# Kernel optimization log

Measured on AMD Instinct MI355X. Metric: run time of the kernel, lower is better.

## Reference

```python
import jax, jax.numpy as jnp
import numpy as np

D_MODEL = 1024
NUM_HEADS = 16
HEAD_DIM = D_MODEL // NUM_HEADS
THETA = 10000.0
BATCH = 2
SEQ = 2048


def _apply_rope(x, positions):
    # x: (b, h, s, hd), positions: (b, s) int
    hd = x.shape[-1]
    inv_freq = 1.0 / (THETA ** (jnp.arange(0, hd, 2, dtype=jnp.float32) / hd))  # (hd/2,)
    ang = positions.astype(jnp.float32)[:, None, :, None] * inv_freq  # (b,1,s,hd/2)
    cos, sin = jnp.cos(ang), jnp.sin(ang)
    x1 = x[..., 0::2]
    x2 = x[..., 1::2]
    r1 = x1 * cos - x2 * sin
    r2 = x1 * sin + x2 * cos
    return jnp.stack([r1, r2], axis=-1).reshape(x.shape)


def setup_inputs() -> dict:
    key = jax.random.key(0)
    ks = jax.random.split(key, 5)
    scale = 1.0 / np.sqrt(D_MODEL)
    x = jax.random.normal(ks[0], (BATCH, SEQ, D_MODEL), dtype=jnp.float32)
    token_positions = jnp.broadcast_to(jnp.arange(SEQ, dtype=jnp.int32), (BATCH, SEQ))
    W_q = jax.random.normal(ks[1], (D_MODEL, D_MODEL), dtype=jnp.float32) * scale
    W_k = jax.random.normal(ks[2], (D_MODEL, D_MODEL), dtype=jnp.float32) * scale
    W_v = jax.random.normal(ks[3], (D_MODEL, D_MODEL), dtype=jnp.float32) * scale
    W_o = jax.random.normal(ks[4], (D_MODEL, D_MODEL), dtype=jnp.float32) * scale
    return {"x": x, "token_positions": token_positions, "W_q": W_q, "W_k": W_k, "W_v": W_v, "W_o": W_o}


def reference(x, token_positions, W_q, W_k, W_v, W_o):
    b, s, _ = x.shape
    h, hd = NUM_HEADS, HEAD_DIM
    # bias-free Linear: y = x @ W^T, W: (out, in)
    def proj(W):
        return jnp.einsum('bsd,ed->bse', x, W).reshape(b, s, h, hd).transpose(0, 2, 1, 3)
    Q = _apply_rope(proj(W_q), token_positions)
    K = _apply_rope(proj(W_k), token_positions)
    V = proj(W_v)
    scores = jnp.einsum('bhqd,bhkd->bhqk', Q, K) / jnp.sqrt(jnp.float32(hd))
    causal = jnp.triu(jnp.full((s, s), -jnp.inf, dtype=scores.dtype), k=1)
    attn = jax.nn.softmax(scores + causal, axis=-1)
    Z = jnp.einsum('bhqk,bhkd->bhqd', attn, V)
    Z = Z.transpose(0, 2, 1, 3).reshape(b, s, h * hd)
    return jnp.einsum('bse,de->bsd', Z, W_o)
```

## Files before the change

kernel.cpp:

```cpp
#include <hip/hip_runtime.h>
#include <hip/hip_bf16.h>


#define BATCH 2
#define SEQ   2048
#define NH    16
#define HD    64
#define DM    1024
#define MTOT  (BATCH*SEQ)

typedef __attribute__((ext_vector_type(8))) short bf16x8;
typedef __attribute__((ext_vector_type(4))) float f32x4;
typedef __attribute__((ext_vector_type(4))) unsigned int u32x4;
typedef unsigned short u16;
typedef unsigned int   u32;

__device__ __forceinline__ float b2f(u16 h){ return __uint_as_float(((u32)h) << 16); }
__device__ __forceinline__ u16 f2b(float f){
  u32 u = __float_as_uint(f);
  u32 r = (u + 0x7FFFu + ((u >> 16) & 1u)) >> 16;
  return (u16)r;
}
__device__ __forceinline__ u16 cvt1(float f){
  __hip_bfloat16 h = __float2bfloat16(f);
  return *reinterpret_cast<u16*>(&h);
}
__device__ __forceinline__ u32 pk2(float lo, float hi){
  return (u32)cvt1(lo) | ((u32)cvt1(hi) << 16);
}
__device__ __forceinline__ f32x4 mfma16(bf16x8 a, bf16x8 b, f32x4 c){
  return __builtin_amdgcn_mfma_f32_16x16x32_bf16(a, b, c, 0, 0, 0);
}
__device__ __forceinline__ void gload_lds16(const u16* g, u16* l){
  __builtin_amdgcn_global_load_lds((const __attribute__((address_space(1))) unsigned int*)g,
                                   (__attribute__((address_space(3))) unsigned int*)l, 16, 0, 0);
}

__global__ __launch_bounds__(256) void cvt_all(const float* __restrict__ x,
    const float* __restrict__ wq, const float* __restrict__ wk,
    const float* __restrict__ wv, const float* __restrict__ wo,
    u16* __restrict__ xb, u16* __restrict__ wb)
{
  const long NX = (long)MTOT * DM;
  const long NW = (long)DM * DM;
  const long tot4 = (NX + 4*NW) >> 2;
  for (long t = (long)blockIdx.x*blockDim.x + threadIdx.x; t < tot4;
       t += (long)gridDim.x*blockDim.x){
    long e = t << 2;
    const float* s; u16* d;
    if (e < NX){ s = x + e; d = xb + e; }
    else {
      long j = e - NX; int z = (int)(j >> 20);
      const float* ws = (z==0)?wq:(z==1)?wk:(z==2)?wv:wo;
      s = ws + (j & (NW-1)); d = wb + j;
    }
    float4 v = *(const float4*)s;
    u32 lo = (u32)f2b(v.x) | ((u32)f2b(v.y) << 16);
    u32 hi = (u32)f2b(v.z) | ((u32)f2b(v.w) << 16);
    uint2 o; o.x = lo; o.y = hi;
    *(uint2*)d = o;
  }
}

__global__ __launch_bounds__(256) void rope_table(float2* __restrict__ tab){
  int t = blockIdx.x*blockDim.x + threadIdx.x;
  if (t >= SEQ*32) return;
  int s = t >> 5, i = t & 31;
  float inv = 1.0f / powf(10000.0f, (float)i * (1.0f/32.0f));
  float a = (float)s * inv;
  tab[t] = make_float2(cosf(a), sinf(a));
}

__device__ __forceinline__ void gemm128_core(const u16* __restrict__ A, const u16* __restrict__ B,
    int mbase, int nbase, u16* Alds, u16* Blds, f32x4 acc[4][4])
{
  const int tid = threadIdx.x;
  const int w = tid >> 6, l = tid & 63, g = l >> 4, c = l & 15;
  const int wr = (w >> 1)*64, wc = (w & 1)*64;
  const int srow = l >> 3;
  const int scol = ((l & 7) ^ srow)*8;
  const u16* Ag = A + (long)(mbase + w*32 + srow)*DM + scol;
  const u16* Bg = B + (long)(nbase + w*32 + srow)*DM + scol;
  u16* Alb = Alds + w*2048;
  u16* Blb = Blds + w*2048;

  for (int k0 = 0; k0 < DM; k0 += 64){
    __syncthreads();
    #pragma unroll
    for (int i = 0; i < 4; i++){
      gload_lds16(Ag + k0 + (long)(8*i)*DM, Alb + i*512);
      gload_lds16(Bg + k0 + (long)(8*i)*DM, Blb + i*512);
    }
    __syncthreads();
    #pragma unroll
    for (int ks = 0; ks < 2; ks++){
      bf16x8 af[4], bfr[4];
      #pragma unroll
      for (int mi = 0; mi < 4; mi++){
        int row = wr + mi*16 + c;
        af[mi] = *(const bf16x8*)&Alds[row*64 + (((ks*4 + g) ^ (row & 7))*8)];
      }
      #pragma unroll
      for (int nj = 0; nj < 4; nj++){
        int row = wc + nj*16 + c;
        bfr[nj] = *(const bf16x8*)&Blds[row*64 + (((ks*4 + g) ^ (row & 7))*8)];
      }
      #pragma unroll
      for (int mi = 0; mi < 4; mi++)
        #pragma unroll
        for (int nj = 0; nj < 4; nj++)
          acc[mi][nj] = mfma16(af[mi], bfr[nj], acc[mi][nj]);
    }
  }
}

__global__ __launch_bounds__(256) void gemm_qkv(const u16* __restrict__ xb,
                                                const u16* __restrict__ wb,
                                                u16* __restrict__ qkvr)
{
  __shared__ u16 Alds[128*64];
  __shared__ u16 Blds[128*64];
  const int z = blockIdx.z;
  const u16* Bm = wb + (long)z * DM * DM;
  u16* C = qkvr + (long)z * MTOT * DM;
  const int nbase = blockIdx.x*128, mbase = blockIdx.y*128;
  const int w = threadIdx.x >> 6, l = threadIdx.x & 63, g = l >> 4, c = l & 15;
  const int wr = (w >> 1)*64, wc = (w & 1)*64;
  f32x4 acc[4][4] = {};
  gemm128_core(xb, Bm, mbase, nbase, Alds, Blds, acc);
  #pragma unroll
  for (int mi = 0; mi < 4; mi++)
    #pragma unroll
    for (int nj = 0; nj < 4; nj++)
      #pragma unroll
      for (int r = 0; r < 4; r++){
        int row = mbase + wr + mi*16 + 4*g + r;
        int col = nbase + wc + nj*16 + c;
        C[(long)row*DM + col] = f2b(acc[mi][nj][r]);
      }
}

__global__ __launch_bounds__(256) void gemm_out(const u16* __restrict__ Zb,
                                                const u16* __restrict__ wob,
                                                float* __restrict__ out)
{
  __shared__ u16 Alds[128*64];
  __shared__ u16 Blds[128*64];
  const int nbase = blockIdx.x*128, mbase = blockIdx.y*128;
  const int w = threadIdx.x >> 6, l = threadIdx.x & 63, g = l >> 4, c = l & 15;
  const int wr = (w >> 1)*64, wc = (w & 1)*64;
  f32x4 acc[4][4] = {};
  gemm128_core(Zb, wob, mbase, nbase, Alds, Blds, acc);
  #pragma unroll
  for (int mi = 0; mi < 4; mi++)
    #pragma unroll
    for (int nj = 0; nj < 4; nj++)
      #pragma unroll
      for (int r = 0; r < 4; r++){
        int row = mbase + wr + mi*16 + 4*g + r;
        int col = nbase + wc + nj*16 + c;
        out[(long)row*DM + col] = acc[mi][nj][r];
      }
}

__global__ __launch_bounds__(256) void rope_scatter(const u16* __restrict__ qkvr,
    u16* __restrict__ Qd, u16* __restrict__ Kd, u16* __restrict__ Vt,
    const float2* __restrict__ tab, const int* __restrict__ pos)
{
  int st = blockIdx.x, h = blockIdx.y, b = blockIdx.z;
  int s0 = st*64;
  const u16* Qraw = qkvr;
  const u16* Kraw = qkvr + (long)MTOT*DM;
  const u16* Vraw = qkvr + 2L*MTOT*DM;
  const float SC = 0.125f * 1.44269504089f;

  for (int t = threadIdx.x; t < 64*32; t += 256){
    int sl = t >> 5, i = t & 31;
    int s = s0 + sl;
    int p = pos[b*SEQ + s];
    if (p < 0) p = 0; if (p >= SEQ) p = SEQ - 1;
    float2 cs = tab[p*32 + i];
    long inoff  = (long)(b*SEQ + s)*DM + h*HD + 2*i;
    long outoff = ((long)(b*NH + h)*SEQ + s)*HD + 2*i;
    u32 qe = *(const u32*)(Qraw + inoff);
    float x1 = b2f((u16)(qe & 0xffff)), x2 = b2f((u16)(qe >> 16));
    float r1 = (x1*cs.x - x2*cs.y)*SC;
    float r2 = (x1*cs.y + x2*cs.x)*SC;
    *(u32*)(Qd + outoff) = (u32)f2b(r1) | ((u32)f2b(r2) << 16);
    u32 ke = *(const u32*)(Kraw + inoff);
    x1 = b2f((u16)(ke & 0xffff)); x2 = b2f((u16)(ke >> 16));
    r1 = x1*cs.x - x2*cs.y;
    r2 = x1*cs.y + x2*cs.x;
    *(u32*)(Kd + outoff) = (u32)f2b(r1) | ((u32)f2b(r2) << 16);
  }

  __shared__ u16 vt[64][65];
  for (int t = threadIdx.x; t < 64*8; t += 256){
    int sl = t >> 3, ch = (t & 7)*8;
    bf16x8 v = *(const bf16x8*)(Vraw + (long)(b*SEQ + s0 + sl)*DM + h*HD + ch);
    #pragma unroll
    for (int j = 0; j < 8; j++) vt[sl][ch + j] = (u16)v[j];
  }
  __syncthreads();
  for (int t = threadIdx.x; t < 64*8; t += 256){
    int d = t >> 3, ch = (t & 7)*8;
    bf16x8 v;
    #pragma unroll
    for (int j = 0; j < 8; j++) v[j] = (short)vt[ch + j][d];
    *(bf16x8*)(Vt + ((long)(b*NH + h)*HD + d)*SEQ + s0 + ch) = v;
  }
}

__device__ __forceinline__ int kperm(int a){
  return (a & 32) | ((a & 4) << 2) | ((a & 24) >> 1) | (a & 3);
}

__global__ __launch_bounds__(256) void attn(const u16* __restrict__ Q, const u16* __restrict__ K,
                                            const u16* __restrict__ Vt,
                                            u16* __restrict__ Opart, float* __restrict__ Lsum)
{
  const int pair = (int)blockIdx.x >> 1;
  const int half = blockIdx.x & 1;
  const int h = blockIdx.y, b = blockIdx.z;
  const int tid = threadIdx.x, w = tid >> 6, l = tid & 63, g = l >> 4, c = l & 15;
  const u16* Kp = K  + (long)(b*NH + h)*SEQ*HD;
  const u16* Vp = Vt + (long)(b*NH + h)*HD*SEQ;

  __shared__ u16 K_lds[2][64][64];
  __shared__ u16 V_lds[2][64][64];

  const int srow0 = tid >> 3, sch = tid & 7;
  const int kpr0 = kperm(srow0), kpr1 = kperm(srow0 + 32);
  const int cswz = c & 7;

  bf16x8 ones;
  #pragma unroll
  for (int j = 0; j < 8; j++) ones[j] = (short)0x3F80;

  int cur = 0;
  #pragma unroll 1
  for (int seg = 0; seg < 2; ++seg){
    const int qt = seg ? (31 - pair) : pair;
    const int qbase = qt*64;
    const int qrow = qbase + w*16;
    const u16* Qp = Q + ((long)(b*NH + h)*SEQ + qrow)*HD;
    bf16x8 qf0 = *(const bf16x8*)(Qp + c*HD + g*8);
    bf16x8 qf1 = *(const bf16x8*)(Qp + c*HD + 32 + g*8);

    const int ntH0  = (qt + 2) >> 1;
    const int tstart = half ? ntH0 : 0;
    const int tend   = half ? (qt + 1) : ntH0;

    f32x4 accz[4] = {};
    f32x4 lacc = {};

    if (tstart < tend){
      __syncthreads();
      bf16x8 kr[2], vr[2];
      #pragma unroll
      for (int i = 0; i < 2; i++){
        int row = srow0 + i*32;
        kr[i] = *(const bf16x8*)(Kp + (long)(tstart*64 + row)*HD + sch*8);
        vr[i] = *(const bf16x8*)(Vp + (long)row*SEQ + tstart*64 + sch*8);
      }
      *(bf16x8*)&K_lds[cur][kpr0][(sch ^ (kpr0 & 7))*8] = kr[0];
      *(bf16x8*)&K_lds[cur][kpr1][(sch ^ (kpr1 & 7))*8] = kr[1];
      *(bf16x8*)&V_lds[cur][srow0][(sch ^ (srow0 & 7))*8] = vr[0];
      *(bf16x8*)&V_lds[cur][srow0+32][(sch ^ ((srow0+32) & 7))*8] = vr[1];

      for (int t = tstart; t < tend; ++t){
        const int kbase = t*64;
        __syncthreads();

        if (t < tend-1){
          const int nb = kbase + 64;
          #pragma unroll
          for (int i = 0; i < 2; i++){
            int row = srow0 + i*32;
            kr[i] = *(const bf16x8*)(Kp + (long)(nb + row)*HD + sch*8);
            vr[i] = *(const bf16x8*)(Vp + (long)row*SEQ + nb + sch*8);
          }
        }

        f32x4 s[4];
        __builtin_amdgcn_s_setprio(1);
        #pragma unroll
        for (int sub = 0; sub < 4; sub++){
          int row = sub*16 + c;
          bf16x8 ka0 = *(const bf16x8*)&K_lds[cur][row][((0+g) ^ cswz)*8];
          bf16x8 ka1 = *(const bf16x8*)&K_lds[cur][row][((4+g) ^ cswz)*8];
          f32x4 z4 = {};
          z4 = mfma16(ka0, qf0, z4);
          z4 = mfma16(ka1, qf1, z4);
          s[sub] = z4;
        }
        __builtin_amdgcn_s_setprio(0);

        const bool edge = (kbase + 63 > qrow);
        const int q = qrow + c;
        if (edge){
          #pragma unroll
          for (int sub = 0; sub < 4; sub++)
            #pragma unroll
            for (int r = 0; r < 4; r++){
              int key = kbase + ((sub >> 1) << 5) + 8*g + ((sub & 1) << 2) + r;
              if (key > q) s[sub][r] = -1e30f;
            }
        }
        #pragma unroll
        for (int sub = 0; sub < 4; sub++)
          #pragma unroll
          for (int r = 0; r < 4; r++)
            s[sub][r] = exp2f(s[sub][r]);

        u32x4 p0, p1;
        p0[0] = pk2(s[0][0], s[0][1]); p0[1] = pk2(s[0][2], s[0][3]);
        p0[2] = pk2(s[1][0], s[1][1]); p0[3] = pk2(s[1][2], s[1][3]);
        p1[0] = pk2(s[2][0], s[2][1]); p1[1] = pk2(s[2][2], s[2][3]);
        p1[2] = pk2(s[3][0], s[3][1]); p1[3] = pk2(s[3][2], s[3][3]);
        bf16x8 pf0 = __builtin_bit_cast(bf16x8, p0);
        bf16x8 pf1 = __builtin_bit_cast(bf16x8, p1);

        __builtin_amdgcn_s_setprio(1);
        lacc = mfma16(pf0, ones, lacc);
        lacc = mfma16(pf1, ones, lacc);
        #pragma unroll
        for (int dt = 0; dt < 4; dt++){
          int vrow = dt*16 + c;
          bf16x8 vf0 = *(const bf16x8*)&V_lds[cur][vrow][((0+g) ^ cswz)*8];
          bf16x8 vf1 = *(const bf16x8*)&V_lds[cur][vrow][((4+g) ^ cswz)*8];
          accz[dt] = mfma16(pf0, vf0, accz[dt]);
          accz[dt] = mfma16(pf1, vf1, accz[dt]);
        }
        __builtin_amdgcn_s_setprio(0);

        if (t < tend-1){
          int nx = cur ^ 1;
          *(bf16x8*)&K_lds[nx][kpr0][(sch ^ (kpr0 & 7))*8] = kr[0];
          *(bf16x8*)&K_lds[nx][kpr1][(sch ^ (kpr1 & 7))*8] = kr[1];
          *(bf16x8*)&V_lds[nx][srow0][(sch ^ (srow0 & 7))*8] = vr[0];
          *(bf16x8*)&V_lds[nx][srow0+32][(sch ^ ((srow0+32) & 7))*8] = vr[1];
          cur = nx;
        }
      }
    }

    const int pbase = (((b*NH + h)*32 + qt)*2 + half);
    if (c == 0){
      #pragma unroll
      for (int r = 0; r < 4; r++)
        Lsum[pbase*64 + w*16 + 4*g + r] = lacc[r];
    }
    u16* Op = Opart + (long)pbase*(64*64);
    #pragma unroll
    for (int dt = 0; dt < 4; dt++)
      #pragma unroll
      for (int r = 0; r < 4; r++)
        Op[(w*16 + 4*g + r)*64 + dt*16 + c] = cvt1(accz[dt][r]);
  }
}

__global__ __launch_bounds__(256) void attn_combine(const u16* __restrict__ Opart,
                                                    const float* __restrict__ Lsum,
                                                    u16* __restrict__ Z)
{
  const int qt = blockIdx.x, h = blockIdx.y, b = blockIdx.z;
  const int p0 = ((b*NH + h)*32 + qt)*2, p1 = p0 + 1;
  const int row = threadIdx.x >> 2;
  const int d0  = (threadIdx.x & 3)*16;
  float inv = 1.f / (Lsum[p0*64 + row] + Lsum[p1*64 + row]);
  const u16* o0 = Opart + ((long)p0*64 + row)*64 + d0;
  const u16* o1 = Opart + ((long)p1*64 + row)*64 + d0;
  const int s = qt*64 + row;
  u16* zp = Z + (long)(b*SEQ + s)*DM + h*HD + d0;
  #pragma unroll
  for (int j = 0; j < 2; j++){
    bf16x8 va = *(const bf16x8*)(o0 + j*8);
    bf16x8 vb = *(const bf16x8*)(o1 + j*8);
    bf16x8 ov;
    #pragma unroll
    for (int e = 0; e < 8; e++){
      float z = (b2f((u16)va[e]) + b2f((u16)vb[e]))*inv;
      ov[e] = (short)cvt1(z);
    }
    *(bf16x8*)(zp + j*8) = ov;
  }
}

extern "C" void kernel_launch(void* const* d_in, const int* in_sizes, int n_in,
                              void* d_out, int out_size, void* d_ws, size_t ws_size,
                              hipStream_t stream)
{
  const float* x  = (const float*)d_in[0];
  const int*   pos= (const int*)d_in[1];
  const float* wq = (const float*)d_in[2];
  const float* wk = (const float*)d_in[3];
  const float* wv = (const float*)d_in[4];
  const float* wo = (const float*)d_in[5];
  float* out = (float*)d_out;

  const long NX = (long)MTOT*DM;
  const long NW = (long)DM*DM;
  char* p = (char*)d_ws;
  u16* xb   = (u16*)p;  p += NX*2;
  u16* wb   = (u16*)p;  p += 4*NW*2;
  u16* qkvr = (u16*)p;  p += 3*NX*2;
  u16* Qd   = (u16*)p;  p += NX*2;
  u16* Kd   = (u16*)p;  p += NX*2;
  u16* Vt   = (u16*)p;  p += NX*2;
  u16* Zb   = (u16*)p;  p += NX*2;
  float2* tab = (float2*)p; p += (long)SEQ*32*sizeof(float2);
  u16* Opart = (u16*)p;  p += 2L*NX*2;
  float* Lsum = (float*)p; p += 2048L*64*sizeof(float);
  (void)ws_size; (void)n_in; (void)in_sizes; (void)out_size;

  hipLaunchKernelGGL(cvt_all,     dim3(2048),      dim3(256), 0, stream, x, wq, wk, wv, wo, xb, wb);
  hipLaunchKernelGGL(rope_table,  dim3(256),       dim3(256), 0, stream, tab);
  hipLaunchKernelGGL(gemm_qkv,    dim3(8,32,3),    dim3(256), 0, stream, xb, wb, qkvr);
  hipLaunchKernelGGL(rope_scatter,dim3(32,16,2),   dim3(256), 0, stream, qkvr, Qd, Kd, Vt, tab, pos);
  hipLaunchKernelGGL(attn,        dim3(32,16,2),   dim3(256), 0, stream, Qd, Kd, Vt, Opart, Lsum);
  hipLaunchKernelGGL(attn_combine,dim3(32,16,2),   dim3(256), 0, stream, Opart, Lsum, Zb);
  hipLaunchKernelGGL(gemm_out,    dim3(8,32),      dim3(256), 0, stream, Zb, wb + 3*NW, out);
}
```

Baseline: 124.6 us.

## Use 128x64 tiles for output GEMM and flatten attention LDS addressing

The output projection GEMM moves from 128x128 tiles to 128x64 tiles with its own inline direct-to-LDS load loop, doubling the grid from 256 to 512 blocks so more CUs are occupied on the 4096x1024 output. Separately, the attention kernel merges its K/V shared buffers into one flat array and uses precomputed offsets and pointer increments in place of per-iteration index arithmetic. The smaller GEMM tile lowers data reuse per block and raises total global traffic.

```diff
diff --git a/kernel.cpp b/kernel.cpp
--- a/kernel.cpp
+++ b/kernel.cpp
@@ -145,16 +145,52 @@
                                                 float* __restrict__ out)
 {
   __shared__ u16 Alds[128*64];
-  __shared__ u16 Blds[128*64];
-  const int nbase = blockIdx.x*128, mbase = blockIdx.y*128;
-  const int w = threadIdx.x >> 6, l = threadIdx.x & 63, g = l >> 4, c = l & 15;
-  const int wr = (w >> 1)*64, wc = (w & 1)*64;
-  f32x4 acc[4][4] = {};
-  gemm128_core(Zb, wob, mbase, nbase, Alds, Blds, acc);
+  __shared__ u16 Blds[64*64];
+  const int nbase = blockIdx.x*64, mbase = blockIdx.y*128;
+  const int tid = threadIdx.x;
+  const int w = tid >> 6, l = tid & 63, g = l >> 4, c = l & 15;
+  const int wr = (w >> 1)*64, wc = (w & 1)*32;
+  const int srow = l >> 3;
+  const int scol = ((l & 7) ^ srow)*8;
+  const u16* Ag = Zb  + (long)(mbase + w*32 + srow)*DM + scol;
+  const u16* Bg = wob + (long)(nbase + w*16 + srow)*DM + scol;
+  u16* Alb = Alds + w*2048;
+  u16* Blb = Blds + w*1024;
+  f32x4 acc[4][2] = {};
+
+  for (int k0 = 0; k0 < DM; k0 += 64){
+    __syncthreads();
+    #pragma unroll
+    for (int i = 0; i < 4; i++)
+      gload_lds16(Ag + k0 + (long)(8*i)*DM, Alb + i*512);
+    #pragma unroll
+    for (int i = 0; i < 2; i++)
+      gload_lds16(Bg + k0 + (long)(8*i)*DM, Blb + i*512);
+    __syncthreads();
+    #pragma unroll
+    for (int ks = 0; ks < 2; ks++){
+      bf16x8 af[4], bfr[2];
+      #pragma unroll
+      for (int mi = 0; mi < 4; mi++){
+        int row = wr + mi*16 + c;
+        af[mi] = *(const bf16x8*)&Alds[row*64 + (((ks*4 + g) ^ (row & 7))*8)];
+      }
+      #pragma unroll
+      for (int nj = 0; nj < 2; nj++){
+        int row = wc + nj*16 + c;
+        bfr[nj] = *(const bf16x8*)&Blds[row*64 + (((ks*4 + g) ^ (row & 7))*8)];
+      }
+      #pragma unroll
+      for (int mi = 0; mi < 4; mi++)
+        #pragma unroll
+        for (int nj = 0; nj < 2; nj++)
+          acc[mi][nj] = mfma16(af[mi], bfr[nj], acc[mi][nj]);
+    }
+  }
   #pragma unroll
   for (int mi = 0; mi < 4; mi++)
     #pragma unroll
-    for (int nj = 0; nj < 4; nj++)
+    for (int nj = 0; nj < 2; nj++)
       #pragma unroll
       for (int r = 0; r < 4; r++){
         int row = mbase + wr + mi*16 + 4*g + r;
@@ -226,18 +262,25 @@
   const u16* Kp = K  + (long)(b*NH + h)*SEQ*HD;
   const u16* Vp = Vt + (long)(b*NH + h)*HD*SEQ;
 
-  __shared__ u16 K_lds[2][64][64];
-  __shared__ u16 V_lds[2][64][64];
+  __shared__ u16 KV[2][2][64][64];
+  u16* kv = &KV[0][0][0][0];
 
   const int srow0 = tid >> 3, sch = tid & 7;
   const int kpr0 = kperm(srow0), kpr1 = kperm(srow0 + 32);
   const int cswz = c & 7;
 
+  const int wk0 = kpr0*64 + (sch ^ (kpr0 & 7))*8;
+  const int wk1 = kpr1*64 + (sch ^ (kpr1 & 7))*8;
+  const int wv0 = 4096 + srow0*64 + (sch ^ (srow0 & 7))*8;
+  const int wv1 = 4096 + (srow0 + 32)*64 + (sch ^ ((srow0 + 32) & 7))*8;
+  const int ra0 = c*64 + (((0 + g) ^ cswz)*8);
+  const int ra1 = c*64 + (((4 + g) ^ cswz)*8);
+
   bf16x8 ones;
   #pragma unroll
   for (int j = 0; j < 8; j++) ones[j] = (short)0x3F80;
 
-  int cur = 0;
+  int bufo = 0;
   #pragma unroll 1
   for (int seg = 0; seg < 2; ++seg){
     const int qt = seg ? (31 - pair) : pair;
@@ -256,39 +299,36 @@
 
     if (tstart < tend){
       __syncthreads();
-      bf16x8 kr[2], vr[2];
-      #pragma unroll
-      for (int i = 0; i < 2; i++){
-        int row = srow0 + i*32;
-        kr[i] = *(const bf16x8*)(Kp + (long)(tstart*64 + row)*HD + sch*8);
-        vr[i] = *(const bf16x8*)(Vp + (long)row*SEQ + tstart*64 + sch*8);
-      }
-      *(bf16x8*)&K_lds[cur][kpr0][(sch ^ (kpr0 & 7))*8] = kr[0];
-      *(bf16x8*)&K_lds[cur][kpr1][(sch ^ (kpr1 & 7))*8] = kr[1];
-      *(bf16x8*)&V_lds[cur][srow0][(sch ^ (srow0 & 7))*8] = vr[0];
-      *(bf16x8*)&V_lds[cur][srow0+32][(sch ^ ((srow0+32) & 7))*8] = vr[1];
+      const u16* kg0 = Kp + (long)(tstart*64 + srow0)*HD + sch*8;
+      const u16* kg1 = kg0 + 32*HD;
+      const u16* vg0 = Vp + (long)srow0*SEQ + tstart*64 + sch*8;
+      const u16* vg1 = vg0 + 32*SEQ;
+      bf16x8 kr0 = *(const bf16x8*)kg0, kr1 = *(const bf16x8*)kg1;
+      bf16x8 vr0 = *(const bf16x8*)vg0, vr1 = *(const bf16x8*)vg1;
+      kg0 += 64*HD; kg1 += 64*HD; vg0 += 64; vg1 += 64;
+      *(bf16x8*)(kv + bufo + wk0) = kr0;
+      *(bf16x8*)(kv + bufo + wk1) = kr1;
+      *(bf16x8*)(kv + bufo + wv0) = vr0;
+      *(bf16x8*)(kv + bufo + wv1) = vr1;
 
       for (int t = tstart; t < tend; ++t){
         const int kbase = t*64;
         __syncthreads();
 
         if (t < tend-1){
-          const int nb = kbase + 64;
-          #pragma unroll
-          for (int i = 0; i < 2; i++){
-            int row = srow0 + i*32;
-            kr[i] = *(const bf16x8*)(Kp + (long)(nb + row)*HD + sch*8);
-            vr[i] = *(const bf16x8*)(Vp + (long)row*SEQ + nb + sch*8);
-          }
+          kr0 = *(const bf16x8*)kg0; kr1 = *(const bf16x8*)kg1;
+          vr0 = *(const bf16x8*)vg0; vr1 = *(const bf16x8*)vg1;
+          kg0 += 64*HD; kg1 += 64*HD; vg0 += 64; vg1 += 64;
         }
+
+        const u16* kvb = kv + bufo;
 
         f32x4 s[4];
         __builtin_amdgcn_s_setprio(1);
         #pragma unroll
         for (int sub = 0; sub < 4; sub++){
-          int row = sub*16 + c;
-          bf16x8 ka0 = *(const bf16x8*)&K_lds[cur][row][((0+g) ^ cswz)*8];
-          bf16x8 ka1 = *(const bf16x8*)&K_lds[cur][row][((4+g) ^ cswz)*8];
+          bf16x8 ka0 = *(const bf16x8*)(kvb + ra0 + sub*1024);
+          bf16x8 ka1 = *(const bf16x8*)(kvb + ra1 + sub*1024);
           f32x4 z4 = {};
           z4 = mfma16(ka0, qf0, z4);
           z4 = mfma16(ka1, qf1, z4);
@@ -326,21 +366,20 @@
         lacc = mfma16(pf1, ones, lacc);
         #pragma unroll
         for (int dt = 0; dt < 4; dt++){
-          int vrow = dt*16 + c;
-          bf16x8 vf0 = *(const bf16x8*)&V_lds[cur][vrow][((0+g) ^ cswz)*8];
-          bf16x8 vf1 = *(const bf16x8*)&V_lds[cur][vrow][((4+g) ^ cswz)*8];
+          bf16x8 vf0 = *(const bf16x8*)(kvb + 4096 + ra0 + dt*1024);
+          bf16x8 vf1 = *(const bf16x8*)(kvb + 4096 + ra1 + dt*1024);
           accz[dt] = mfma16(pf0, vf0, accz[dt]);
           accz[dt] = mfma16(pf1, vf1, accz[dt]);
         }
         __builtin_amdgcn_s_setprio(0);
 
         if (t < tend-1){
-          int nx = cur ^ 1;
-          *(bf16x8*)&K_lds[nx][kpr0][(sch ^ (kpr0 & 7))*8] = kr[0];
-          *(bf16x8*)&K_lds[nx][kpr1][(sch ^ (kpr1 & 7))*8] = kr[1];
-          *(bf16x8*)&V_lds[nx][srow0][(sch ^ (srow0 & 7))*8] = vr[0];
-          *(bf16x8*)&V_lds[nx][srow0+32][(sch ^ ((srow0+32) & 7))*8] = vr[1];
-          cur = nx;
+          int nbo = bufo ^ 8192;
+          *(bf16x8*)(kv + nbo + wk0) = kr0;
+          *(bf16x8*)(kv + nbo + wk1) = kr1;
+          *(bf16x8*)(kv + nbo + wv0) = vr0;
+          *(bf16x8*)(kv + nbo + wv1) = vr1;
+          bufo = nbo;
         }
       }
     }
@@ -420,5 +459,5 @@
   hipLaunchKernelGGL(rope_scatter,dim3(32,16,2),   dim3(256), 0, stream, qkvr, Qd, Kd, Vt, tab, pos);
   hipLaunchKernelGGL(attn,        dim3(32,16,2),   dim3(256), 0, stream, Qd, Kd, Vt, Opart, Lsum);
   hipLaunchKernelGGL(attn_combine,dim3(32,16,2),   dim3(256), 0, stream, Opart, Lsum, Zb);
-  hipLaunchKernelGGL(gemm_out,    dim3(8,32),      dim3(256), 0, stream, Zb, wb + 3*NW, out);
-}
+  hipLaunchKernelGGL(gemm_out,    dim3(16,32),     dim3(256), 0, stream, Zb, wb + 3*NW, out);
+}
```

New measurement: 119.7 us. 1.04x faster.
